# Performance work log

Measured on AMD Instinct MI355X. Metric: run time of the kernel, lower is better.

Reference implementation:

```python
import jax, jax.numpy as jnp
import numpy as np

B, N, D = 2, 2048, 1024
H, HD = 16, 64            # num_heads, head_dim
INNER = H * HD
EPS = 1e-5


def setup_inputs() -> dict:
    key = jax.random.key(0)
    k0, k1, k2, k3 = jax.random.split(key, 4)
    x = jax.random.normal(k0, (B, N, D), dtype=jnp.float32)
    attn_mask = jax.random.randint(k1, (B, N, N), 0, 2, dtype=jnp.int32)
    gamma = jnp.ones((D,), jnp.float32)
    beta = jnp.zeros((D,), jnp.float32)
    w_qkv = jax.random.normal(k2, (D, 3 * INNER), dtype=jnp.float32) * 0.02
    w_out = jax.random.normal(k3, (INNER, D), dtype=jnp.float32) * 0.02
    b_out = jnp.zeros((D,), jnp.float32)
    return {"x": x, "attn_mask": attn_mask, "gamma": gamma, "beta": beta,
            "w_qkv": w_qkv, "w_out": w_out, "b_out": b_out}


def _rope_tables(n):
    # RotaryEmbedding buffers: sin/cos of shape [n, HD//2]
    inv_freq = 1.0 / (10000.0 ** (jnp.arange(0, HD, 2, dtype=jnp.float32) / HD))
    pos = jnp.arange(n, dtype=jnp.float32)
    ang = pos[:, None] * inv_freq[None, :]          # [n, HD//2]
    return jnp.sin(ang), jnp.cos(ang)


def _apply_rope(t, sin, cos):
    # t: [B, H, N, HD]; sin/cos broadcast as [1, 1, N, HD//2]
    t1, t2 = t[..., : HD // 2], t[..., HD // 2:]
    return jnp.concatenate([t1 * cos - t2 * sin, t2 * cos + t1 * sin], axis=-1)


def reference(x, attn_mask, gamma, beta, w_qkv, w_out, b_out):
    b, n, _ = x.shape
    # LayerNorm
    mu = jnp.mean(x, axis=-1, keepdims=True)
    var = jnp.mean(jnp.square(x - mu), axis=-1, keepdims=True)
    xn = (x - mu) * jax.lax.rsqrt(var + EPS) * gamma + beta
    # QKV projection (no bias)
    qkv = xn @ w_qkv                                 # [B, N, 3*INNER]
    q, k, v = jnp.split(qkv, 3, axis=-1)
    def to_heads(t):
        return t.reshape(b, n, H, HD).transpose(0, 2, 1, 3)  # [B, H, N, HD]
    q, k, v = to_heads(q), to_heads(k), to_heads(v)
    sin, cos = _rope_tables(n)
    sin = sin[None, None]                            # [1,1,N,HD//2]
    cos = cos[None, None]
    q = _apply_rope(q, sin, cos)
    k = _apply_rope(k, sin, cos)
    scale = HD ** -0.5
    scores = jnp.einsum('bhid,bhjd->bhij', q, k) * scale
    mask = (attn_mask > 0)[:, None, :, :]            # [B,1,N,N]
    scores = jnp.where(mask, scores, -jnp.inf)
    probs = jax.nn.softmax(scores, axis=-1)
    probs = jnp.nan_to_num(probs, nan=0.0)           # rows fully masked -> 0
    out = jnp.einsum('bhij,bhjd->bhid', probs, v)    # [B,H,N,HD]
    out = out.transpose(0, 2, 1, 3).reshape(b, n, INNER)
    return out @ w_out + b_out
```

## Files before the change

kernel.cpp:

```cpp
#include <hip/hip_runtime.h>
#include <stdint.h>
#include <math.h>

#define B_ 2
#define N_ 2048
#define D_ 1024
#define H_ 16
#define HD_ 64
#define TOK (B_*N_)
#define INNER_ (H_*HD_)

typedef unsigned short u16;
typedef __attribute__((ext_vector_type(8))) short bf16x8;
typedef __attribute__((ext_vector_type(4))) float f32x4;

__device__ __forceinline__ float bf2f(u16 u) {
  union { uint32_t i; float f; } v; v.i = ((uint32_t)u) << 16; return v.f;
}
__device__ __forceinline__ u16 f2bf(float f) {
  union { uint32_t i; float f; } v; v.f = f;
  uint32_t r = ((v.i >> 16) & 1u) + 0x7fffu;
  return (u16)((v.i + r) >> 16);
}
__device__ __forceinline__ uint32_t pk_trunc(float a, float b) {
  return __builtin_amdgcn_perm(__float_as_uint(b), __float_as_uint(a), 0x07060302);
}
__device__ __forceinline__ uint32_t pk_rnd(float a, float b) {
  uint32_t ua = __float_as_uint(a) + 0x8000u;
  uint32_t ub = __float_as_uint(b) + 0x8000u;
  return __builtin_amdgcn_perm(ub, ua, 0x07060302);
}
__device__ __forceinline__ void gl_lds16(const void* g, void* l) {
  __builtin_amdgcn_global_load_lds(
      (const __attribute__((address_space(1))) uint32_t*)g,
      (__attribute__((address_space(3))) uint32_t*)l, 16, 0, 0);
}
__device__ __forceinline__ f32x4 mfma16(bf16x8 a, bf16x8 b, f32x4 c) {
  return __builtin_amdgcn_mfma_f32_16x16x32_bf16(a, b, c, 0, 0, 0);
}

__global__ void pack_mask(const int* __restrict__ mask, uint64_t* __restrict__ bits) {
  int t = threadIdx.x, lane = t & 63, w = t >> 6;
  int seg = blockIdx.x * 4 + w;
  int row = seg >> 3, s = seg & 7;
  const int* mp = mask + (size_t)row * 2048 + s * 256;
  int b = row >> 11, i = row & 2047;
  uint64_t* bp = bits + (size_t)b * 32 * 2048 + i;
  for (int j = 0; j < 4; j++) {
    int m = mp[j * 64 + lane];
    uint64_t bm = __ballot(m > 0);
    if (lane == 0) bp[(size_t)(s * 4 + j) * 2048] = bm;
  }
}

__global__ void rtab_kernel(float2* __restrict__ rtab) {
  int i = blockIdx.x * 256 + threadIdx.x;
  int pos = i >> 5, p = i & 31;
  float inv = exp2f(-(float)p * (13.287712379549449f / 32.0f));
  float sn, cs;
  sincosf((float)pos * inv, &sn, &cs);
  rtab[i] = make_float2(sn, cs);
}

__global__ void transpose_f2b(const float* __restrict__ in, u16* __restrict__ out,
                              int R, int C) {
  __shared__ u16 tile[64][65];
  int c0 = blockIdx.x * 64, r0 = blockIdx.y * 64;
  int t = threadIdx.x;
  int c = t & 63, r4 = t >> 6;
  for (int i = 0; i < 16; i++) {
    int r = r4 + i * 4;
    tile[c][r] = f2bf(in[(size_t)(r0 + r) * C + c0 + c]);
  }
  __syncthreads();
  int rr = t & 63, cc4 = t >> 6;
  for (int i = 0; i < 16; i++) {
    int cc = cc4 + i * 4;
    out[(size_t)(c0 + cc) * R + r0 + rr] = tile[cc][rr];
  }
}

__global__ void ln_kernel(const float* __restrict__ x, const float* __restrict__ gamma,
                          const float* __restrict__ beta, u16* __restrict__ xn) {
  int row = blockIdx.x, t = threadIdx.x;
  const float* xr = x + (size_t)row * D_;
  float4 u = *(const float4*)(xr + t * 4);
  float s = u.x + u.y + u.z + u.w;
  float ss = u.x * u.x + u.y * u.y + u.z * u.z + u.w * u.w;
  for (int off = 1; off < 64; off <<= 1) {
    s += __shfl_xor(s, off);
    ss += __shfl_xor(ss, off);
  }
  __shared__ float red[8];
  int wid = t >> 6, lane = t & 63;
  if (lane == 0) { red[wid] = s; red[wid + 4] = ss; }
  __syncthreads();
  s = red[0] + red[1] + red[2] + red[3];
  ss = red[4] + red[5] + red[6] + red[7];
  float mu = s * (1.0f / D_);
  float var = ss * (1.0f / D_) - mu * mu;
  float rinv = rsqrtf(var + 1e-5f);
  float4 g4 = *(const float4*)(gamma + t * 4);
  float4 b4 = *(const float4*)(beta + t * 4);
  ushort4 o;
  o.x = f2bf((u.x - mu) * rinv * g4.x + b4.x);
  o.y = f2bf((u.y - mu) * rinv * g4.y + b4.y);
  o.z = f2bf((u.z - mu) * rinv * g4.z + b4.z);
  o.w = f2bf((u.w - mu) * rinv * g4.w + b4.w);
  *(ushort4*)(xn + (size_t)row * D_ + t * 4) = o;
}

__global__ void gemm_qkv(const u16* __restrict__ A, const u16* __restrict__ Bt,
                         const float2* __restrict__ rtab,
                         u16* __restrict__ q, u16* __restrict__ k,
                         u16* __restrict__ vt) {
  const int K = 1024;
  __shared__ __align__(16) u16 As[128 * 64];
  __shared__ __align__(16) u16 Bs[128 * 64];
  const int t = threadIdx.x;
  const int lane = t & 63, wid = t >> 6;
  const int m0 = blockIdx.y * 128, n0 = blockIdx.x * 128;
  const int wm = (wid >> 1) * 64, wn = (wid & 1) * 64;
  const int l15 = lane & 15, quad = lane >> 4;

  f32x4 acc[4][4];
  const f32x4 zf = {0.f, 0.f, 0.f, 0.f};
  for (int i = 0; i < 4; i++) for (int j = 0; j < 4; j++) acc[i][j] = zf;

  for (int kb = 0; kb < K; kb += 64) {
    for (int i = 0; i < 4; i++) {
      int e = i * 256 + t;
      int row = e >> 3, gs = e & 7;
      int g = gs ^ (row & 7);
      gl_lds16(A + (size_t)(m0 + row) * K + kb + g * 8, &As[e * 8]);
      gl_lds16(Bt + (size_t)(n0 + row) * K + kb + g * 8, &Bs[e * 8]);
    }
    __syncthreads();
    bf16x8 af[4][2], bfr[4][2];
    for (int mt = 0; mt < 4; mt++)
      for (int kc = 0; kc < 2; kc++) {
        int row = wm + mt * 16 + l15;
        int gs = (kc * 4 + quad) ^ (row & 7);
        af[mt][kc] = *(const bf16x8*)&As[row * 64 + gs * 8];
      }
    for (int nt = 0; nt < 4; nt++)
      for (int kc = 0; kc < 2; kc++) {
        int row = wn + nt * 16 + l15;
        int gs = (kc * 4 + quad) ^ (row & 7);
        bfr[nt][kc] = *(const bf16x8*)&Bs[row * 64 + gs * 8];
      }
    for (int mt = 0; mt < 4; mt++)
      for (int nt = 0; nt < 4; nt++)
        for (int kc = 0; kc < 2; kc++)
          acc[mt][nt] = mfma16(af[mt][kc], bfr[nt][kc], acc[mt][nt]);
    __syncthreads();
  }

  const int sec = n0 >> 10;
  const int h = ((n0 & 1023) >> 6) + (wn >> 6);
  if (sec < 2) {
    u16* dst = sec ? k : q;
    const float scale = sec ? 1.0f : 0.125f * 1.4426950408889634f;
    for (int mt = 0; mt < 4; mt++)
      for (int r = 0; r < 4; r++) {
        int row = m0 + wm + mt * 16 + quad * 4 + r;
        int b = row >> 11, pos = row & 2047;
        float2 c0 = rtab[pos * 32 + l15];
        float2 c1 = rtab[pos * 32 + 16 + l15];
        float a0 = acc[mt][0][r], a1 = acc[mt][1][r];
        float a2 = acc[mt][2][r], a3 = acc[mt][3][r];
        float o0 = (a0 * c0.y - a2 * c0.x) * scale;
        float o2 = (a2 * c0.y + a0 * c0.x) * scale;
        float o1 = (a1 * c1.y - a3 * c1.x) * scale;
        float o3 = (a3 * c1.y + a1 * c1.x) * scale;
        size_t base = ((size_t)(b * 16 + h) * 2048 + pos) * 64;
        dst[base + l15]      = f2bf(o0);
        dst[base + 16 + l15] = f2bf(o1);
        dst[base + 32 + l15] = f2bf(o2);
        dst[base + 48 + l15] = f2bf(o3);
      }
  } else {
    for (int mt = 0; mt < 4; mt++) {
      int u = (wm + mt * 16) >> 4;
      int c = (u >> 1) & 1, hi = u & 1;
      int rowb = m0 + (u >> 2) * 64;
      int b = rowb >> 11, nb = rowb & 2047;
      int slot = nb + c * 32 + quad * 8 + hi * 4;
      for (int nt = 0; nt < 4; nt++) {
        int d = nt * 16 + l15;
        size_t base = ((size_t)(b * 16 + h) * 64 + d) * 2048 + slot;
        uint2 o;
        o.x = pk_rnd(acc[mt][nt][0], acc[mt][nt][1]);
        o.y = pk_rnd(acc[mt][nt][2], acc[mt][nt][3]);
        *(uint2*)&vt[base] = o;
      }
    }
  }
}

__global__ void gemm_out(const u16* __restrict__ A, const u16* __restrict__ Bt,
                         float* __restrict__ C, const float* __restrict__ bias) {
  const int N = 1024, K = 1024;
  __shared__ __align__(16) u16 As[2][128 * 64];
  __shared__ __align__(16) u16 Bs[2][128 * 64];
  const int t = threadIdx.x;
  const int lane = t & 63, wid = t >> 6;
  const int m0 = blockIdx.y * 128, n0 = blockIdx.x * 128;
  const int wm = (wid >> 1) * 64, wn = (wid & 1) * 64;
  const int l15 = lane & 15, quad = lane >> 4;

  f32x4 acc[4][4];
  const f32x4 zf = {0.f, 0.f, 0.f, 0.f};
  for (int i = 0; i < 4; i++) for (int j = 0; j < 4; j++) acc[i][j] = zf;

  for (int i = 0; i < 4; i++) {
    int e = i * 256 + t;
    int row = e >> 3, gs = e & 7, g = gs ^ (row & 7);
    gl_lds16(A + (size_t)(m0 + row) * K + g * 8, &As[0][e * 8]);
    gl_lds16(Bt + (size_t)(n0 + row) * K + g * 8, &Bs[0][e * 8]);
  }
  for (int ki = 0; ki < 16; ki++) {
    int cur = ki & 1;
    __syncthreads();
    if (ki + 1 < 16) {
      int nxt = cur ^ 1, kb = (ki + 1) * 64;
      for (int i = 0; i < 4; i++) {
        int e = i * 256 + t;
        int row = e >> 3, gs = e & 7, g = gs ^ (row & 7);
        gl_lds16(A + (size_t)(m0 + row) * K + kb + g * 8, &As[nxt][e * 8]);
        gl_lds16(Bt + (size_t)(n0 + row) * K + kb + g * 8, &Bs[nxt][e * 8]);
      }
    }
    bf16x8 af[4][2], bfr[4][2];
    for (int mt = 0; mt < 4; mt++)
      for (int kc = 0; kc < 2; kc++) {
        int row = wm + mt * 16 + l15;
        int gs = (kc * 4 + quad) ^ (row & 7);
        af[mt][kc] = *(const bf16x8*)&As[cur][row * 64 + gs * 8];
      }
    for (int nt = 0; nt < 4; nt++)
      for (int kc = 0; kc < 2; kc++) {
        int row = wn + nt * 16 + l15;
        int gs = (kc * 4 + quad) ^ (row & 7);
        bfr[nt][kc] = *(const bf16x8*)&Bs[cur][row * 64 + gs * 8];
      }
    for (int mt = 0; mt < 4; mt++)
      for (int nt = 0; nt < 4; nt++)
        for (int kc = 0; kc < 2; kc++)
          acc[mt][nt] = mfma16(af[mt][kc], bfr[nt][kc], acc[mt][nt]);
  }
  for (int mt = 0; mt < 4; mt++)
    for (int nt = 0; nt < 4; nt++)
      for (int r = 0; r < 4; r++) {
        int row = m0 + wm + mt * 16 + quad * 4 + r;
        int col = n0 + wn + nt * 16 + l15;
        C[(size_t)row * N + col] = acc[mt][nt][r] + bias[col];
      }
}

__global__ __launch_bounds__(256, 4)
void attn_kernel(const u16* __restrict__ q, const u16* __restrict__ k,
                 const u16* __restrict__ vt, const uint64_t* __restrict__ bitsT,
                 u16* __restrict__ out) {
  int blk = blockIdx.x;
  int qt = blk & 31;
  int bh = blk >> 5;
  int b = bh >> 4, h = bh & 15;
  int q0 = qt * 64;
  int t = threadIdx.x, lane = t & 63, w = t >> 6;
  int l15 = lane & 15, quad = lane >> 4;

  __shared__ __align__(16) u16 sQ[64 * 64];
  __shared__ __align__(16) u16 sK[2][64 * 64];
  __shared__ __align__(16) u16 sV[2][64 * 64];

  {
    int e0 = t, e1 = 256 + t;
    int r0 = e0 >> 3, g0 = (e0 & 7) ^ (r0 & 7);
    int r1 = e1 >> 3, g1 = (e1 & 7) ^ (r1 & 7);
    gl_lds16(q + ((size_t)bh * 2048 + q0 + r0) * 64 + g0 * 8, &sQ[e0 * 8]);
    gl_lds16(q + ((size_t)bh * 2048 + q0 + r1) * 64 + g1 * 8, &sQ[e1 * 8]);
    gl_lds16(k + ((size_t)bh * 2048 + r0) * 64 + g0 * 8, &sK[0][e0 * 8]);
    gl_lds16(k + ((size_t)bh * 2048 + r1) * 64 + g1 * 8, &sK[0][e1 * 8]);
    gl_lds16(vt + ((size_t)bh * 64 + r0) * 2048 + g0 * 8, &sV[0][e0 * 8]);
    gl_lds16(vt + ((size_t)bh * 64 + r1) * 2048 + g1 * 8, &sV[0][e1 * 8]);
  }
  __syncthreads();

  bf16x8 bq[2];
  {
    int row = w * 16 + l15;
    for (int kc = 0; kc < 2; kc++) {
      int gs = (kc * 4 + quad) ^ (row & 7);
      bq[kc] = *(const bf16x8*)&sQ[row * 64 + gs * 8];
    }
  }

  const f32x4 zf = {0.f, 0.f, 0.f, 0.f};
  float l_i = 0.f;
  f32x4 acc_o[4];
  for (int dt = 0; dt < 4; dt++) acc_o[dt] = zf;
  const int qrow = q0 + w * 16 + l15;

  #pragma unroll 2
  for (int j64 = 0; j64 < 32; j64++) {
    if (j64) __syncthreads();
    int cur = j64 & 1;
    if (j64 + 1 < 32) {
      int nxt = cur ^ 1, j0n = (j64 + 1) * 64;
      int e0 = t, e1 = 256 + t;
      int r0 = e0 >> 3, g0 = (e0 & 7) ^ (r0 & 7);
      int r1 = e1 >> 3, g1 = (e1 & 7) ^ (r1 & 7);
      gl_lds16(k + ((size_t)bh * 2048 + j0n + r0) * 64 + g0 * 8, &sK[nxt][e0 * 8]);
      gl_lds16(k + ((size_t)bh * 2048 + j0n + r1) * 64 + g1 * 8, &sK[nxt][e1 * 8]);
      gl_lds16(vt + ((size_t)bh * 64 + r0) * 2048 + j0n + g0 * 8, &sV[nxt][e0 * 8]);
      gl_lds16(vt + ((size_t)bh * 64 + r1) * 2048 + j0n + g1 * 8, &sV[nxt][e1 * 8]);
    }
    const u16* sKc = sK[cur];
    const u16* sVc = sV[cur];

    uint64_t word = bitsT[((size_t)(b * 32 + j64)) * 2048 + qrow];
    uint64_t sh = word >> (quad * 4);
    uint32_t mlo = (uint32_t)sh, mhi = (uint32_t)(sh >> 32);

    float p[16];
    {
      f32x4 st[4];
      for (int jt = 0; jt < 4; jt++) {
        st[jt] = zf;
        int row = jt * 16 + l15;
        for (int kc = 0; kc < 2; kc++) {
          int gs = (kc * 4 + quad) ^ (row & 7);
          bf16x8 ak = *(const bf16x8*)&sKc[row * 64 + gs * 8];
          st[jt] = mfma16(ak, bq[kc], st[jt]);
        }
      }
      for (int jt = 0; jt < 4; jt++) {
        uint32_t mw = (jt & 2) ? mhi : mlo;
        int base = (jt & 1) * 16;
        for (int r = 0; r < 4; r++) {
          bool on = (mw >> (base + r)) & 1u;
          float e = exp2f(st[jt][r]);
          p[jt * 4 + r] = on ? e : 0.f;
        }
      }
    }
    float rsum = 0.f;
    for (int i = 0; i < 16; i++) rsum += p[i];
    rsum += __shfl_xor(rsum, 16);
    rsum += __shfl_xor(rsum, 32);
    l_i += rsum;

    for (int c = 0; c < 2; c++) {
      union { bf16x8 v; uint32_t d[4]; } bp;
      bp.d[0] = pk_trunc(p[(2 * c) * 4 + 0], p[(2 * c) * 4 + 1]);
      bp.d[1] = pk_trunc(p[(2 * c) * 4 + 2], p[(2 * c) * 4 + 3]);
      bp.d[2] = pk_trunc(p[(2 * c + 1) * 4 + 0], p[(2 * c + 1) * 4 + 1]);
      bp.d[3] = pk_trunc(p[(2 * c + 1) * 4 + 2], p[(2 * c + 1) * 4 + 3]);
      for (int dt = 0; dt < 4; dt++) {
        int drow = dt * 16 + l15;
        int gpos = (4 * c + quad) ^ (drow & 7);
        bf16x8 av = *(const bf16x8*)&sVc[drow * 64 + gpos * 8];
        acc_o[dt] = mfma16(av, bp.v, acc_o[dt]);
      }
    }
  }
  float rl = (l_i > 0.f) ? 1.0f / l_i : 0.f;
  size_t obase = ((size_t)b * 2048 + qrow) * 1024 + h * 64;
  for (int dt = 0; dt < 4; dt++) {
    ushort4 o;
    o.x = f2bf(acc_o[dt][0] * rl);
    o.y = f2bf(acc_o[dt][1] * rl);
    o.z = f2bf(acc_o[dt][2] * rl);
    o.w = f2bf(acc_o[dt][3] * rl);
    *(ushort4*)&out[obase + dt * 16 + quad * 4] = o;
  }
}

extern "C" void kernel_launch(void* const* d_in, const int* in_sizes, int n_in,
                              void* d_out, int out_size, void* d_ws, size_t ws_size,
                              hipStream_t stream) {
  const float* x = (const float*)d_in[0];
  const int* mask = (const int*)d_in[1];
  const float* gamma = (const float*)d_in[2];
  const float* beta = (const float*)d_in[3];
  const float* wqkv = (const float*)d_in[4];
  const float* wout = (const float*)d_in[5];
  const float* bout = (const float*)d_in[6];
  float* out = (float*)d_out;

  uint8_t* ws = (uint8_t*)d_ws;
  size_t o = 0;
  uint64_t* mbits = (uint64_t*)(ws + o); o += (size_t)TOK * 32 * 8;
  u16* wqkvT = (u16*)(ws + o); o += (size_t)3 * INNER_ * D_ * 2;
  u16* woutT = (u16*)(ws + o); o += (size_t)INNER_ * D_ * 2;
  u16* xn    = (u16*)(ws + o); o += (size_t)TOK * D_ * 2;
  u16* qb    = (u16*)(ws + o); o += (size_t)TOK * INNER_ * 2;
  u16* kb    = (u16*)(ws + o); o += (size_t)TOK * INNER_ * 2;
  u16* vtb   = (u16*)(ws + o); o += (size_t)TOK * INNER_ * 2;
  u16* ao    = (u16*)(ws + o); o += (size_t)TOK * INNER_ * 2;
  float2* rtab = (float2*)(ws + o); o += (size_t)2048 * 32 * 8;

  pack_mask<<<8192, 256, 0, stream>>>(mask, mbits);
  rtab_kernel<<<256, 256, 0, stream>>>(rtab);
  transpose_f2b<<<dim3(3 * INNER_ / 64, D_ / 64), 256, 0, stream>>>(wqkv, wqkvT, D_, 3 * INNER_);
  transpose_f2b<<<dim3(D_ / 64, INNER_ / 64), 256, 0, stream>>>(wout, woutT, INNER_, D_);
  ln_kernel<<<TOK, 256, 0, stream>>>(x, gamma, beta, xn);
  gemm_qkv<<<dim3(3 * INNER_ / 128, TOK / 128), 256, 0, stream>>>(xn, wqkvT, rtab, qb, kb, vtb);
  attn_kernel<<<B_ * H_ * (N_ / 64), 256, 0, stream>>>(qb, kb, vtb, mbits, ao);
  gemm_out<<<dim3(D_ / 128, TOK / 128), 256, 0, stream>>>(ao, woutT, out, bout);
}
```

Measured before the change: 247.2 us.

## Merge prep kernels, pre-swizzle Q/K tiles, and shrink gemm_out M tile

Five preprocessing launches (mask packing, rope table, two weight transposes, layernorm) are merged into one kernel that picks its role from the block index, cutting launch overhead and idle tails. gemm_qkv now stages rotated Q/K through LDS and writes them as contiguous, pre-swizzled 64x64 tiles, so attention loads them as plain linear 16-byte copies. gemm_out uses a 64-row M tile, doubling the grid to improve occupancy and wave balance across the CUs. The cost is an extra LDS round trip and barrier in the Q/K epilogue, plus a branchier prep kernel.

Measured after the change: 229.8 us. 7.0% less time.

```diff
diff --git a/kernel.cpp b/kernel.cpp
--- a/kernel.cpp
+++ b/kernel.cpp
@@ -39,75 +39,78 @@
   return __builtin_amdgcn_mfma_f32_16x16x32_bf16(a, b, c, 0, 0, 0);
 }
 
-__global__ void pack_mask(const int* __restrict__ mask, uint64_t* __restrict__ bits) {
-  int t = threadIdx.x, lane = t & 63, w = t >> 6;
-  int seg = blockIdx.x * 4 + w;
-  int row = seg >> 3, s = seg & 7;
-  const int* mp = mask + (size_t)row * 2048 + s * 256;
-  int b = row >> 11, i = row & 2047;
-  uint64_t* bp = bits + (size_t)b * 32 * 2048 + i;
-  for (int j = 0; j < 4; j++) {
-    int m = mp[j * 64 + lane];
-    uint64_t bm = __ballot(m > 0);
-    if (lane == 0) bp[(size_t)(s * 4 + j) * 2048] = bm;
-  }
-}
-
-__global__ void rtab_kernel(float2* __restrict__ rtab) {
-  int i = blockIdx.x * 256 + threadIdx.x;
-  int pos = i >> 5, p = i & 31;
-  float inv = exp2f(-(float)p * (13.287712379549449f / 32.0f));
-  float sn, cs;
-  sincosf((float)pos * inv, &sn, &cs);
-  rtab[i] = make_float2(sn, cs);
-}
-
-__global__ void transpose_f2b(const float* __restrict__ in, u16* __restrict__ out,
-                              int R, int C) {
+__global__ void prep_kernel(const float* __restrict__ x, const float* __restrict__ gamma,
+                            const float* __restrict__ beta, u16* __restrict__ xn,
+                            const float* __restrict__ wqkv, u16* __restrict__ wqkvT,
+                            const float* __restrict__ wout, u16* __restrict__ woutT,
+                            const int* __restrict__ mask, uint64_t* __restrict__ bits,
+                            float2* __restrict__ rtab) {
   __shared__ u16 tile[64][65];
-  int c0 = blockIdx.x * 64, r0 = blockIdx.y * 64;
-  int t = threadIdx.x;
-  int c = t & 63, r4 = t >> 6;
-  for (int i = 0; i < 16; i++) {
-    int r = r4 + i * 4;
-    tile[c][r] = f2bf(in[(size_t)(r0 + r) * C + c0 + c]);
-  }
-  __syncthreads();
-  int rr = t & 63, cc4 = t >> 6;
-  for (int i = 0; i < 16; i++) {
-    int cc = cc4 + i * 4;
-    out[(size_t)(c0 + cc) * R + r0 + rr] = tile[cc][rr];
-  }
-}
-
-__global__ void ln_kernel(const float* __restrict__ x, const float* __restrict__ gamma,
-                          const float* __restrict__ beta, u16* __restrict__ xn) {
-  int row = blockIdx.x, t = threadIdx.x;
-  const float* xr = x + (size_t)row * D_;
-  float4 u = *(const float4*)(xr + t * 4);
-  float s = u.x + u.y + u.z + u.w;
-  float ss = u.x * u.x + u.y * u.y + u.z * u.z + u.w * u.w;
-  for (int off = 1; off < 64; off <<= 1) {
-    s += __shfl_xor(s, off);
-    ss += __shfl_xor(ss, off);
-  }
   __shared__ float red[8];
-  int wid = t >> 6, lane = t & 63;
-  if (lane == 0) { red[wid] = s; red[wid + 4] = ss; }
-  __syncthreads();
-  s = red[0] + red[1] + red[2] + red[3];
-  ss = red[4] + red[5] + red[6] + red[7];
-  float mu = s * (1.0f / D_);
-  float var = ss * (1.0f / D_) - mu * mu;
-  float rinv = rsqrtf(var + 1e-5f);
-  float4 g4 = *(const float4*)(gamma + t * 4);
-  float4 b4 = *(const float4*)(beta + t * 4);
-  ushort4 o;
-  o.x = f2bf((u.x - mu) * rinv * g4.x + b4.x);
-  o.y = f2bf((u.y - mu) * rinv * g4.y + b4.y);
-  o.z = f2bf((u.z - mu) * rinv * g4.z + b4.z);
-  o.w = f2bf((u.w - mu) * rinv * g4.w + b4.w);
-  *(ushort4*)(xn + (size_t)row * D_ + t * 4) = o;
+  int blk = blockIdx.x, t = threadIdx.x;
+  if (blk < 4096) {
+    int row = blk;
+    const float* xr = x + (size_t)row * D_;
+    float4 u = *(const float4*)(xr + t * 4);
+    float s = u.x + u.y + u.z + u.w;
+    float ss = u.x * u.x + u.y * u.y + u.z * u.z + u.w * u.w;
+    for (int off = 1; off < 64; off <<= 1) {
+      s += __shfl_xor(s, off);
+      ss += __shfl_xor(ss, off);
+    }
+    int wid = t >> 6, lane = t & 63;
+    if (lane == 0) { red[wid] = s; red[wid + 4] = ss; }
+    __syncthreads();
+    s = red[0] + red[1] + red[2] + red[3];
+    ss = red[4] + red[5] + red[6] + red[7];
+    float mu = s * (1.0f / D_);
+    float var = ss * (1.0f / D_) - mu * mu;
+    float rinv = rsqrtf(var + 1e-5f);
+    float4 g4 = *(const float4*)(gamma + t * 4);
+    float4 b4 = *(const float4*)(beta + t * 4);
+    ushort4 o;
+    o.x = f2bf((u.x - mu) * rinv * g4.x + b4.x);
+    o.y = f2bf((u.y - mu) * rinv * g4.y + b4.y);
+    o.z = f2bf((u.z - mu) * rinv * g4.z + b4.z);
+    o.w = f2bf((u.w - mu) * rinv * g4.w + b4.w);
+    *(ushort4*)(xn + (size_t)row * D_ + t * 4) = o;
+  } else if (blk < 5120) {
+    const float* in; u16* outp; int R, C, bx, by;
+    if (blk < 4864) { int idx = blk - 4096; in = wqkv; outp = wqkvT; R = 1024; C = 3072; bx = idx % 48; by = idx / 48; }
+    else            { int idx = blk - 4864; in = wout; outp = woutT; R = 1024; C = 1024; bx = idx % 16; by = idx / 16; }
+    int c0 = bx * 64, r0 = by * 64;
+    int c = t & 63, r4 = t >> 6;
+    for (int i = 0; i < 16; i++) {
+      int r = r4 + i * 4;
+      tile[c][r] = f2bf(in[(size_t)(r0 + r) * C + c0 + c]);
+    }
+    __syncthreads();
+    int rr = t & 63, cc4 = t >> 6;
+    for (int i = 0; i < 16; i++) {
+      int cc = cc4 + i * 4;
+      outp[(size_t)(c0 + cc) * R + r0 + rr] = tile[cc][rr];
+    }
+  } else if (blk < 13312) {
+    int idx = blk - 5120;
+    int lane = t & 63, w = t >> 6;
+    int seg = idx * 4 + w;
+    int row = seg >> 3, s = seg & 7;
+    const int* mp = mask + (size_t)row * 2048 + s * 256;
+    int b = row >> 11, i = row & 2047;
+    uint64_t* bp = bits + (size_t)b * 32 * 2048 + i;
+    for (int j = 0; j < 4; j++) {
+      int m = mp[j * 64 + lane];
+      uint64_t bm = __ballot(m > 0);
+      if (lane == 0) bp[(size_t)(s * 4 + j) * 2048] = bm;
+    }
+  } else {
+    int i = (blk - 13312) * 256 + t;
+    int pos = i >> 5, p = i & 31;
+    float inv = exp2f(-(float)p * (13.287712379549449f / 32.0f));
+    float sn, cs;
+    sincosf((float)pos * inv, &sn, &cs);
+    rtab[i] = make_float2(sn, cs);
+  }
 }
 
 __global__ void gemm_qkv(const u16* __restrict__ A, const u16* __restrict__ Bt,
@@ -115,8 +118,9 @@
                          u16* __restrict__ q, u16* __restrict__ k,
                          u16* __restrict__ vt) {
   const int K = 1024;
-  __shared__ __align__(16) u16 As[128 * 64];
-  __shared__ __align__(16) u16 Bs[128 * 64];
+  __shared__ __align__(16) u16 smem[16384];
+  u16* As = smem;
+  u16* Bs = smem + 8192;
   const int t = threadIdx.x;
   const int lane = t & 63, wid = t >> 6;
   const int m0 = blockIdx.y * 128, n0 = blockIdx.x * 128;
@@ -157,38 +161,53 @@
   }
 
   const int sec = n0 >> 10;
-  const int h = ((n0 & 1023) >> 6) + (wn >> 6);
+  const int h_base = (n0 & 1023) >> 6;
   if (sec < 2) {
     u16* dst = sec ? k : q;
     const float scale = sec ? 1.0f : 0.125f * 1.4426950408889634f;
+    const int img = (wn >> 6) * 2 + (wm >> 6);
+    u16* im = smem + img * 4096;
     for (int mt = 0; mt < 4; mt++)
       for (int r = 0; r < 4; r++) {
-        int row = m0 + wm + mt * 16 + quad * 4 + r;
-        int b = row >> 11, pos = row & 2047;
+        int lr = mt * 16 + quad * 4 + r;
+        int rowg = m0 + wm + lr;
+        int pos = rowg & 2047;
         float2 c0 = rtab[pos * 32 + l15];
         float2 c1 = rtab[pos * 32 + 16 + l15];
         float a0 = acc[mt][0][r], a1 = acc[mt][1][r];
         float a2 = acc[mt][2][r], a3 = acc[mt][3][r];
         float o0 = (a0 * c0.y - a2 * c0.x) * scale;
+        float o1 = (a1 * c1.y - a3 * c1.x) * scale;
         float o2 = (a2 * c0.y + a0 * c0.x) * scale;
-        float o1 = (a1 * c1.y - a3 * c1.x) * scale;
         float o3 = (a3 * c1.y + a1 * c1.x) * scale;
-        size_t base = ((size_t)(b * 16 + h) * 2048 + pos) * 64;
-        dst[base + l15]      = f2bf(o0);
-        dst[base + 16 + l15] = f2bf(o1);
-        dst[base + 32 + l15] = f2bf(o2);
-        dst[base + 48 + l15] = f2bf(o3);
-      }
+        int rx = lr & 7, dl = l15 & 7, dh = l15 >> 3;
+        int base = lr * 64;
+        im[base + ((0 + dh) ^ rx) * 8 + dl] = f2bf(o0);
+        im[base + ((2 + dh) ^ rx) * 8 + dl] = f2bf(o1);
+        im[base + ((4 + dh) ^ rx) * 8 + dl] = f2bf(o2);
+        im[base + ((6 + dh) ^ rx) * 8 + dl] = f2bf(o3);
+      }
+    __syncthreads();
+    for (int i = 0; i < 8; i++) {
+      int u = i * 2048 + t * 8;
+      int ig = u >> 12, off = u & 4095;
+      int hh = ig >> 1, tt = ig & 1;
+      int rowg0 = m0 + tt * 64;
+      int bb = rowg0 >> 11;
+      int tl = (rowg0 & 2047) >> 6;
+      size_t base = ((size_t)(bb * 16 + h_base + hh) * 32 + tl) * 4096 + off;
+      *(uint4*)&dst[base] = *(const uint4*)&smem[u];
+    }
   } else {
+    const int h = h_base + (wn >> 6);
     for (int mt = 0; mt < 4; mt++) {
-      int u = (wm + mt * 16) >> 4;
-      int c = (u >> 1) & 1, hi = u & 1;
-      int rowb = m0 + (u >> 2) * 64;
-      int b = rowb >> 11, nb = rowb & 2047;
-      int slot = nb + c * 32 + quad * 8 + hi * 4;
+      int tb = wm + mt * 16;
+      int bb = (m0 + tb) >> 11;
+      int n64 = ((m0 + tb) & 2047) & ~63;
+      int slot = n64 + (tb & 32) + ((tb & 16) >> 2) + quad * 8;
       for (int nt = 0; nt < 4; nt++) {
         int d = nt * 16 + l15;
-        size_t base = ((size_t)(b * 16 + h) * 64 + d) * 2048 + slot;
+        size_t base = ((size_t)(bb * 16 + h) * 64 + d) * 2048 + slot;
         uint2 o;
         o.x = pk_rnd(acc[mt][nt][0], acc[mt][nt][1]);
         o.y = pk_rnd(acc[mt][nt][2], acc[mt][nt][3]);
@@ -201,38 +220,48 @@
 __global__ void gemm_out(const u16* __restrict__ A, const u16* __restrict__ Bt,
                          float* __restrict__ C, const float* __restrict__ bias) {
   const int N = 1024, K = 1024;
-  __shared__ __align__(16) u16 As[2][128 * 64];
+  __shared__ __align__(16) u16 As[2][64 * 64];
   __shared__ __align__(16) u16 Bs[2][128 * 64];
   const int t = threadIdx.x;
   const int lane = t & 63, wid = t >> 6;
-  const int m0 = blockIdx.y * 128, n0 = blockIdx.x * 128;
-  const int wm = (wid >> 1) * 64, wn = (wid & 1) * 64;
+  const int m0 = blockIdx.y * 64, n0 = blockIdx.x * 128;
+  const int wm = (wid >> 1) * 32, wn = (wid & 1) * 64;
   const int l15 = lane & 15, quad = lane >> 4;
 
-  f32x4 acc[4][4];
+  f32x4 acc[2][4];
   const f32x4 zf = {0.f, 0.f, 0.f, 0.f};
-  for (int i = 0; i < 4; i++) for (int j = 0; j < 4; j++) acc[i][j] = zf;
-
-  for (int i = 0; i < 4; i++) {
-    int e = i * 256 + t;
-    int row = e >> 3, gs = e & 7, g = gs ^ (row & 7);
-    gl_lds16(A + (size_t)(m0 + row) * K + g * 8, &As[0][e * 8]);
-    gl_lds16(Bt + (size_t)(n0 + row) * K + g * 8, &Bs[0][e * 8]);
+  for (int i = 0; i < 2; i++) for (int j = 0; j < 4; j++) acc[i][j] = zf;
+
+  {
+    for (int i = 0; i < 2; i++) {
+      int e = i * 256 + t;
+      int row = e >> 3, gs = e & 7, g = gs ^ (row & 7);
+      gl_lds16(A + (size_t)(m0 + row) * K + g * 8, &As[0][e * 8]);
+    }
+    for (int i = 0; i < 4; i++) {
+      int e = i * 256 + t;
+      int row = e >> 3, gs = e & 7, g = gs ^ (row & 7);
+      gl_lds16(Bt + (size_t)(n0 + row) * K + g * 8, &Bs[0][e * 8]);
+    }
   }
   for (int ki = 0; ki < 16; ki++) {
     int cur = ki & 1;
     __syncthreads();
     if (ki + 1 < 16) {
       int nxt = cur ^ 1, kb = (ki + 1) * 64;
+      for (int i = 0; i < 2; i++) {
+        int e = i * 256 + t;
+        int row = e >> 3, gs = e & 7, g = gs ^ (row & 7);
+        gl_lds16(A + (size_t)(m0 + row) * K + kb + g * 8, &As[nxt][e * 8]);
+      }
       for (int i = 0; i < 4; i++) {
         int e = i * 256 + t;
         int row = e >> 3, gs = e & 7, g = gs ^ (row & 7);
-        gl_lds16(A + (size_t)(m0 + row) * K + kb + g * 8, &As[nxt][e * 8]);
         gl_lds16(Bt + (size_t)(n0 + row) * K + kb + g * 8, &Bs[nxt][e * 8]);
       }
     }
-    bf16x8 af[4][2], bfr[4][2];
-    for (int mt = 0; mt < 4; mt++)
+    bf16x8 af[2][2], bfr[4][2];
+    for (int mt = 0; mt < 2; mt++)
       for (int kc = 0; kc < 2; kc++) {
         int row = wm + mt * 16 + l15;
         int gs = (kc * 4 + quad) ^ (row & 7);
@@ -244,12 +273,12 @@
         int gs = (kc * 4 + quad) ^ (row & 7);
         bfr[nt][kc] = *(const bf16x8*)&Bs[cur][row * 64 + gs * 8];
       }
-    for (int mt = 0; mt < 4; mt++)
+    for (int mt = 0; mt < 2; mt++)
       for (int nt = 0; nt < 4; nt++)
         for (int kc = 0; kc < 2; kc++)
           acc[mt][nt] = mfma16(af[mt][kc], bfr[nt][kc], acc[mt][nt]);
   }
-  for (int mt = 0; mt < 4; mt++)
+  for (int mt = 0; mt < 2; mt++)
     for (int nt = 0; nt < 4; nt++)
       for (int r = 0; r < 4; r++) {
         int row = m0 + wm + mt * 16 + quad * 4 + r;
@@ -276,12 +305,14 @@
 
   {
     int e0 = t, e1 = 256 + t;
+    const u16* qim = q + ((size_t)bh * 32 + qt) * 4096;
+    const u16* kim = k + (size_t)bh * 32 * 4096;
+    gl_lds16(qim + e0 * 8, &sQ[e0 * 8]);
+    gl_lds16(qim + e1 * 8, &sQ[e1 * 8]);
+    gl_lds16(kim + e0 * 8, &sK[0][e0 * 8]);
+    gl_lds16(kim + e1 * 8, &sK[0][e1 * 8]);
     int r0 = e0 >> 3, g0 = (e0 & 7) ^ (r0 & 7);
     int r1 = e1 >> 3, g1 = (e1 & 7) ^ (r1 & 7);
-    gl_lds16(q + ((size_t)bh * 2048 + q0 + r0) * 64 + g0 * 8, &sQ[e0 * 8]);
-    gl_lds16(q + ((size_t)bh * 2048 + q0 + r1) * 64 + g1 * 8, &sQ[e1 * 8]);
-    gl_lds16(k + ((size_t)bh * 2048 + r0) * 64 + g0 * 8, &sK[0][e0 * 8]);
-    gl_lds16(k + ((size_t)bh * 2048 + r1) * 64 + g1 * 8, &sK[0][e1 * 8]);
     gl_lds16(vt + ((size_t)bh * 64 + r0) * 2048 + g0 * 8, &sV[0][e0 * 8]);
     gl_lds16(vt + ((size_t)bh * 64 + r1) * 2048 + g1 * 8, &sV[0][e1 * 8]);
   }
@@ -309,10 +340,11 @@
     if (j64 + 1 < 32) {
       int nxt = cur ^ 1, j0n = (j64 + 1) * 64;
       int e0 = t, e1 = 256 + t;
+      const u16* kim = k + ((size_t)bh * 32 + j64 + 1) * 4096;
+      gl_lds16(kim + e0 * 8, &sK[nxt][e0 * 8]);
+      gl_lds16(kim + e1 * 8, &sK[nxt][e1 * 8]);
       int r0 = e0 >> 3, g0 = (e0 & 7) ^ (r0 & 7);
       int r1 = e1 >> 3, g1 = (e1 & 7) ^ (r1 & 7);
-      gl_lds16(k + ((size_t)bh * 2048 + j0n + r0) * 64 + g0 * 8, &sK[nxt][e0 * 8]);
-      gl_lds16(k + ((size_t)bh * 2048 + j0n + r1) * 64 + g1 * 8, &sK[nxt][e1 * 8]);
       gl_lds16(vt + ((size_t)bh * 64 + r0) * 2048 + j0n + g0 * 8, &sV[nxt][e0 * 8]);
       gl_lds16(vt + ((size_t)bh * 64 + r1) * 2048 + j0n + g1 * 8, &sV[nxt][e1 * 8]);
     }
@@ -401,12 +433,9 @@
   u16* ao    = (u16*)(ws + o); o += (size_t)TOK * INNER_ * 2;
   float2* rtab = (float2*)(ws + o); o += (size_t)2048 * 32 * 8;
 
-  pack_mask<<<8192, 256, 0, stream>>>(mask, mbits);
-  rtab_kernel<<<256, 256, 0, stream>>>(rtab);
-  transpose_f2b<<<dim3(3 * INNER_ / 64, D_ / 64), 256, 0, stream>>>(wqkv, wqkvT, D_, 3 * INNER_);
-  transpose_f2b<<<dim3(D_ / 64, INNER_ / 64), 256, 0, stream>>>(wout, woutT, INNER_, D_);
-  ln_kernel<<<TOK, 256, 0, stream>>>(x, gamma, beta, xn);
+  prep_kernel<<<13568, 256, 0, stream>>>(x, gamma, beta, xn, wqkv, wqkvT,
+                                         wout, woutT, mask, mbits, rtab);
   gemm_qkv<<<dim3(3 * INNER_ / 128, TOK / 128), 256, 0, stream>>>(xn, wqkvT, rtab, qb, kb, vtb);
   attn_kernel<<<B_ * H_ * (N_ / 64), 256, 0, stream>>>(qb, kb, vtb, mbits, ao);
-  gemm_out<<<dim3(D_ / 128, TOK / 128), 256, 0, stream>>>(ao, woutT, out, bout);
-}
+  gemm_out<<<dim3(D_ / 128, TOK / 64), 256, 0, stream>>>(ao, woutT, out, bout);
+}
```
